# Kernel tuning notes

Hardware: AMD Instinct MI355X
Metric: run time of the kernel (lower is better)

Reference implementation:

```python
import jax, jax.numpy as jnp
import numpy as np
from jax import lax

B, N, C = 256, 256, 192
HEADS = 6
HD = C // HEADS
WIN = 16
AGENT = 49
POOL = 7            # int(agent_num ** 0.5)
SCALE = HD ** -0.5


def _pool_matrix(inn, out):
    # PyTorch AdaptiveAvgPool2d bin edges: start=floor(i*inn/out), end=ceil((i+1)*inn/out)
    P = np.zeros((out, inn), np.float32)
    for i in range(out):
        s = (i * inn) // out
        e = -(((-(i + 1)) * inn) // out)
        P[i, s:e] = 1.0 / (e - s)
    return jnp.asarray(P)

_P = _pool_matrix(WIN, POOL)  # (7, 16) adaptive-avg-pool operator


def _resize_bilinear(x, out_h, out_w):
    # matches F.interpolate(mode='bilinear', align_corners=False)
    H, W = x.shape[-2], x.shape[-1]
    def idx(out, inn):
        s = (jnp.arange(out, dtype=jnp.float32) + 0.5) * (inn / out) - 0.5
        s = jnp.maximum(s, 0.0)
        i0 = jnp.minimum(jnp.floor(s).astype(jnp.int32), inn - 1)
        i1 = jnp.minimum(i0 + 1, inn - 1)
        return i0, i1, s - i0.astype(jnp.float32)
    h0, h1, th = idx(out_h, H)
    w0, w1, tw = idx(out_w, W)
    xh = x[..., h0, :] * (1.0 - th)[:, None] + x[..., h1, :] * th[:, None]
    return xh[..., :, w0] * (1.0 - tw) + xh[..., :, w1] * tw


def setup_inputs() -> dict:
    key = jax.random.key(0)
    ks = jax.random.split(key, 18)
    lin = lambda k: jax.random.normal(k, (C, C), jnp.float32) * 0.02
    zc = jnp.zeros((C,), jnp.float32)
    tn = lambda k, shp: jax.random.normal(k, shp, jnp.float32) * 0.02
    return {
        "x_F1": jax.random.normal(ks[0], (B, N, C), jnp.float32),
        "x_C2": jax.random.normal(ks[1], (B, N, C), jnp.float32),
        "x_C1": jax.random.normal(ks[2], (B, N, C), jnp.float32),
        "Wq": lin(ks[3]), "bq": zc,
        "Wk": lin(ks[4]), "bk": zc,
        "Wv": lin(ks[5]), "bv": zc,
        "Wa1": lin(ks[6]), "ba1": zc,
        "Wa2": lin(ks[7]), "ba2": zc,
        "an_bias": tn(ks[8], (HEADS, AGENT, 7, 7)),
        "na_bias": tn(ks[9], (HEADS, AGENT, 7, 7)),
        "ah_bias": tn(ks[10], (1, HEADS, AGENT, WIN, 1)),
        "aw_bias": tn(ks[11], (1, HEADS, AGENT, 1, WIN)),
        "ha_bias": tn(ks[12], (1, HEADS, WIN, 1, AGENT)),
        "wa_bias": tn(ks[13], (1, HEADS, 1, WIN, AGENT)),
        "dwc_w": tn(ks[14], (C, 1, 3, 3)),
        "dwc_b": zc,
        "Wp": lin(ks[15]), "bp": zc,
    }


def reference(x_F1, x_C2, x_C1, Wq, bq, Wk, bk, Wv, bv, Wa1, ba1, Wa2, ba2,
              an_bias, na_bias, ah_bias, aw_bias, ha_bias, wa_bias,
              dwc_w, dwc_b, Wp, bp):
    b, n, c = x_F1.shape
    h = w = WIN
    q = x_F1 @ Wq.T + bq
    k = (x_F1 + x_C2 - x_C1) @ Wk.T + bk
    v = (x_C2 - x_C1) @ Wv.T + bv
    # agent tokens: linear -> adaptive avg pool 16x16 -> 7x7 -> (b, 49, c)
    a1 = (x_C1 @ Wa1.T + ba1).reshape(b, h, w, c)
    a1 = jnp.einsum('ph,bhwc,qw->bpqc', _P, a1, _P).reshape(b, AGENT, c)
    a2 = (x_C2 @ Wa2.T + ba2).reshape(b, h, w, c)
    a2 = jnp.einsum('ph,bhwc,qw->bpqc', _P, a2, _P).reshape(b, AGENT, c)
    qh = q.reshape(b, n, HEADS, HD).transpose(0, 2, 1, 3)
    kh = k.reshape(b, n, HEADS, HD).transpose(0, 2, 1, 3)
    vh = v.reshape(b, n, HEADS, HD).transpose(0, 2, 1, 3)
    a1h = a1.reshape(b, AGENT, HEADS, HD).transpose(0, 2, 1, 3)
    a2h = a2.reshape(b, AGENT, HEADS, HD).transpose(0, 2, 1, 3)
    # stage 1: agent <- k/v attention, bias = interp(an_bias) + (ah+aw)
    pb = (_resize_bilinear(an_bias, h, w).reshape(1, HEADS, AGENT, n)
          + (ah_bias + aw_bias).reshape(1, HEADS, AGENT, n))
    attn2 = jax.nn.softmax(SCALE * jnp.einsum('bhad,bhnd->bhan', a2h, kh) + pb, axis=-1)
    agent_v = jnp.einsum('bhan,bhnd->bhad', attn2, vh)
    # stage 2: query <- agent attention, bias = interp(na_bias)^T + (ha+wa)
    ab = (jnp.swapaxes(_resize_bilinear(na_bias, h, w).reshape(HEADS, AGENT, n), -1, -2)[None]
          + (ha_bias + wa_bias).reshape(1, HEADS, n, AGENT))
    q_attn = jax.nn.softmax(SCALE * jnp.einsum('bhnd,bhad->bhna', qh, a1h) + ab, axis=-1)
    x = jnp.einsum('bhna,bhad->bhnd', q_attn, agent_v).transpose(0, 2, 1, 3).reshape(b, n, c)
    # depthwise 3x3 conv on q as spatial map
    q_img = q.reshape(b, h, w, c).transpose(0, 3, 1, 2)
    dw = lax.conv_general_dilated(q_img, dwc_w, (1, 1), ((1, 1), (1, 1)),
                                  feature_group_count=c,
                                  dimension_numbers=('NCHW', 'OIHW', 'NCHW'))
    dw = dw + dwc_b.reshape(1, c, 1, 1)
    x = x + dw.transpose(0, 2, 3, 1).reshape(b, n, c)
    return x @ Wp.T + bp
```

## Files before the change

### kernel.cpp

```cpp
#include <hip/hip_runtime.h>

typedef __bf16 bf16;
typedef __bf16 bf16x8 __attribute__((ext_vector_type(8)));
typedef float  f32x4  __attribute__((ext_vector_type(4)));

#define DEVI __device__ __forceinline__

static constexpr int   BATCH = 256;
static constexpr int   SEQ   = 256;
static constexpr int   CH    = 192;
static constexpr int   NH    = 6;
static constexpr int   AG    = 49;
static constexpr float QK_SCALE = 0.17677669529663687f;

__device__ constexpr int   PPN[16]  = {1,1,2,1,2,1,2,1,1,2,1,2,1,2,1,1};
__device__ constexpr int   PPB0[16] = {0,0,0,1,1,2,2,3,3,3,4,4,5,5,6,6};
__device__ constexpr int   PPB1[16] = {0,0,1,0,2,0,3,0,0,4,0,5,0,6,0,0};
__device__ constexpr float PPW0[16] = {1.f/3.f,1.f/3.f,1.f/3.f,1.f/3.f,1.f/3.f,1.f/3.f,1.f/3.f,0.25f,0.25f,0.25f,
                                       1.f/3.f,1.f/3.f,1.f/3.f,1.f/3.f,1.f/3.f,1.f/3.f};
__device__ constexpr float PPW1[16] = {0.f,0.f,1.f/3.f,0.f,1.f/3.f,0.f,0.25f,0.f,0.f,1.f/3.f,
                                       0.f,1.f/3.f,0.f,1.f/3.f,0.f,0.f};

#if defined(__has_builtin)
#if __has_builtin(__builtin_amdgcn_global_load_lds)
#define HAVE_GLL 1
#endif
#endif

DEVI void gll16(const void* g, void* l, int lane) {
#ifdef HAVE_GLL
  (void)lane;
  __builtin_amdgcn_global_load_lds(
      (const __attribute__((address_space(1))) void*)g,
      (__attribute__((address_space(3))) void*)l, 16, 0, 0);
#else
  *(uint4*)((char*)l + lane * 16) = *(const uint4*)((const char*)g);
#endif
}

DEVI float bilin7(const float* m, int i, int j) {
  float sh = (i + 0.5f) * 0.4375f - 0.5f; sh = sh < 0.f ? 0.f : sh;
  float sw = (j + 0.5f) * 0.4375f - 0.5f; sw = sw < 0.f ? 0.f : sw;
  int i0 = (int)sh; if (i0 > 6) i0 = 6;
  int j0 = (int)sw; if (j0 > 6) j0 = 6;
  int i1 = i0 + 1;  if (i1 > 6) i1 = 6;
  int j1 = j0 + 1;  if (j1 > 6) j1 = 6;
  float th = sh - (float)i0, tw = sw - (float)j0;
  float v00 = m[i0*7 + j0], v01 = m[i0*7 + j1];
  float v10 = m[i1*7 + j0], v11 = m[i1*7 + j1];
  return (v00*(1.f-tw) + v01*tw)*(1.f-th) + (v10*(1.f-tw) + v11*tw)*th;
}

__global__ void k_prep(const float* Wq, const float* Wk, const float* Wv,
                       const float* Wa1, const float* Wa2, const float* Wp,
                       const float* an_bias, const float* na_bias,
                       const float* ah_bias, const float* aw_bias,
                       const float* ha_bias, const float* wa_bias,
                       bf16* wsW, float* pb, float* ab, bf16* a1, bf16* a2) {
  int gid = blockIdx.x * 256 + threadIdx.x;
  if (gid < 221184) {
    int mi = gid / 36864, r = gid - mi * 36864;
    const float* W = (mi == 0 ? Wq : mi == 1 ? Wk : mi == 2 ? Wv :
                      mi == 3 ? Wa1 : mi == 4 ? Wa2 : Wp);
    wsW[gid] = (bf16)W[r];
  } else if (gid < 296448) {
    int r = gid - 221184;
    int n = r & 255, ha = r >> 8;
    int i = n >> 4, j = n & 15;
    float val = bilin7(an_bias + (size_t)ha * 49, i, j)
              + ah_bias[ha * 16 + i] + aw_bias[ha * 16 + j];
    pb[r] = val;
  } else if (gid < 371712) {
    int r = gid - 296448;
    int a = r % 49, hn = r / 49;
    int n = hn & 255, hh = hn >> 8;
    int i = n >> 4, j = n & 15;
    float val = bilin7(na_bias + (size_t)(hh * 49 + a) * 49, i, j)
              + ha_bias[(hh * 16 + i) * 49 + a] + wa_bias[(hh * 16 + j) * 49 + a];
    ab[r] = val;
  } else if (gid < 396288) {
    int r = gid - 371712;
    if (r < 12288) a1[(size_t)12544 * CH + r] = (bf16)0.f;
    else           a2[(size_t)12544 * CH + (r - 12288)] = (bf16)0.f;
  }
}

__global__ __launch_bounds__(256) void k_combo(
    const float* xF1, const float* xC2, const float* xC1,
    bf16* f1b, bf16* kin, bf16* vin) {
  const int base = blockIdx.x * 768;
  #pragma unroll
  for (int s = 0; s < 3; ++s) {
    const int slot = base + threadIdx.x + 256 * s;
    const int row  = slot / 24;
    const int cb   = slot - row * 24;
    const size_t rf = (size_t)row * CH + cb * 8;
    float f[8], c2[8], c1[8];
    *(float4*)&f[0]  = *(const float4*)(xF1 + rf);
    *(float4*)&f[4]  = *(const float4*)(xF1 + rf + 4);
    *(float4*)&c2[0] = *(const float4*)(xC2 + rf);
    *(float4*)&c2[4] = *(const float4*)(xC2 + rf + 4);
    *(float4*)&c1[0] = *(const float4*)(xC1 + rf);
    *(float4*)&c1[4] = *(const float4*)(xC1 + rf + 4);
    bf16x8 tq, tk, tv;
    #pragma unroll
    for (int e = 0; e < 8; ++e) {
      const float d = c2[e] - c1[e];
      tq[e] = (bf16)f[e];
      tk[e] = (bf16)(f[e] + d);
      tv[e] = (bf16)d;
    }
    const size_t rowb = (size_t)row * 384;
    const int    byt  = (cb * 16) ^ ((row & 7) << 4);
    *(bf16x8*)((char*)f1b + rowb + byt) = tq;
    *(bf16x8*)((char*)kin + rowb + byt) = tk;
    *(bf16x8*)((char*)vin + rowb + byt) = tv;
  }
}

__global__ __launch_bounds__(192) void k_pool(
    const float* xC1, const float* xC2, bf16* pooled1, bf16* pooled2) {
  const int b = blockIdx.x, which = blockIdx.y, c = threadIdx.x;
  const float* src = (which ? xC2 : xC1) + (size_t)b * SEQ * CH + c;
  bf16* dst = (which ? pooled2 : pooled1) + (size_t)b * AG * CH + c;
  float acc[49];
  #pragma unroll
  for (int a = 0; a < 49; ++a) acc[a] = 0.f;
  #pragma unroll
  for (int i = 0; i < 16; ++i) {
    float jq[7] = {0.f, 0.f, 0.f, 0.f, 0.f, 0.f, 0.f};
    #pragma unroll
    for (int j = 0; j < 16; ++j) {
      const float x = src[(i * 16 + j) * CH];
      jq[PPB0[j]] += PPW0[j] * x;
      if (PPN[j] == 2) jq[PPB1[j]] += PPW1[j] * x;
    }
    {
      const int p0 = PPB0[i]; const float w0 = PPW0[i];
      #pragma unroll
      for (int qq = 0; qq < 7; ++qq) acc[p0 * 7 + qq] += w0 * jq[qq];
    }
    if (PPN[i] == 2) {
      const int p1 = PPB1[i]; const float w1 = PPW1[i];
      #pragma unroll
      for (int qq = 0; qq < 7; ++qq) acc[p1 * 7 + qq] += w1 * jq[qq];
    }
  }
  #pragma unroll
  for (int a = 0; a < 49; ++a) dst[(size_t)a * CH + c] = (bf16)acc[a];
}

__global__ __launch_bounds__(256, 3) void k_gemm3b(
    const bf16* f1b, const bf16* kin, const bf16* vin, const bf16* wsW,
    const float* bq, const float* bk, const float* bv,
    bf16* qO, bf16* kO, bf16* vO) {
  __shared__ char sA[49152] __attribute__((aligned(16)));
  const int tid = threadIdx.x, lane = tid & 63, wid = tid >> 6;
  const int l15 = lane & 15, lg = lane >> 4;
  const int wr = wid >> 1, wc = wid & 1;
  const int job = blockIdx.y;
  const int m0 = blockIdx.x * 128;
  const bf16*  Aj   = (job == 0 ? f1b : job == 1 ? kin : vin);
  const bf16*  Wj   = wsW + job * 36864;
  const float* bias = (job == 0 ? bq : job == 1 ? bk : bv);
  bf16*        outp = (job == 0 ? qO : job == 1 ? kO : vO);

  {
    const char* gsrc = (const char*)Aj + (size_t)m0 * 384;
    #pragma unroll
    for (int i = 0; i < 12; ++i) {
      const int off = (wid * 12 + i) * 1024;
      gll16(gsrc + off + lane * 16, sA + off, lane);
    }
  }
  __syncthreads();

  f32x4 acc[4][6];
  #pragma unroll
  for (int a = 0; a < 4; ++a)
    #pragma unroll
    for (int b2 = 0; b2 < 6; ++b2) acc[a][b2] = f32x4{0.f, 0.f, 0.f, 0.f};

  #pragma unroll
  for (int kk = 0; kk < 6; ++kk) {
    bf16x8 af[4];
    #pragma unroll
    for (int rt = 0; rt < 4; ++rt) {
      const int row = 64 * wr + 16 * rt + l15;
      af[rt] = *(const bf16x8*)(sA + row * 384 + ((kk * 64 + lg * 16) ^ ((row & 7) << 4)));
    }
    #pragma unroll
    for (int ct = 0; ct < 6; ++ct) {
      const int ncol = 96 * wc + 16 * ct + l15;
      bf16x8 bfr = *(const bf16x8*)&Wj[(size_t)ncol * CH + kk * 32 + 8 * lg];
      #pragma unroll
      for (int rt = 0; rt < 4; ++rt)
        acc[rt][ct] = __builtin_amdgcn_mfma_f32_16x16x32_bf16(af[rt], bfr, acc[rt][ct], 0, 0, 0);
    }
  }
  __syncthreads();
  #pragma unroll
  for (int ct = 0; ct < 6; ++ct) {
    const int col = 96 * wc + 16 * ct + l15;
    const float bb = bias[col];
    #pragma unroll
    for (int rt = 0; rt < 4; ++rt)
      #pragma unroll
      for (int r = 0; r < 4; ++r) {
        const int row = 64 * wr + 16 * rt + 4 * lg + r;
        *(bf16*)(sA + row * 384 + ((2 * col) ^ ((row & 7) << 4))) = (bf16)(acc[rt][ct][r] + bb);
      }
  }
  __syncthreads();
  #pragma unroll
  for (int g = 0; g < 12; ++g) {
    const int ch  = tid + 256 * g;
    const int row = ch / 24;
    const int y   = (ch - row * 24) * 16;
    bf16x8 vv = *(const bf16x8*)(sA + row * 384 + (y ^ ((row & 7) << 4)));
    *(bf16x8*)((char*)outp + (size_t)(m0 + row) * 384 + y) = vv;
  }
}

DEVI void gemm_body(const bf16* Asrc, const bf16* W, const float* bias,
                    bf16* outp, int m0, bf16 (*sA)[72]) {
  const int tid = threadIdx.x, lane = tid & 63, wid = tid >> 6;
  const int l15 = lane & 15, lg = lane >> 4;
  const int wr = wid >> 1, wc = wid & 1;
  const int srow = tid >> 1, shalf = tid & 1;

  f32x4 acc[4][6];
  #pragma unroll
  for (int a = 0; a < 4; ++a)
    #pragma unroll
    for (int b2 = 0; b2 < 6; ++b2) acc[a][b2] = f32x4{0.f, 0.f, 0.f, 0.f};

  for (int ks = 0; ks < 3; ++ks) {
    const int k0 = ks * 64;
    const uint4* src = (const uint4*)(Asrc + (size_t)(m0 + srow) * CH + k0 + shalf * 32);
    #pragma unroll
    for (int i2 = 0; i2 < 4; ++i2)
      *(uint4*)&sA[srow][shalf * 32 + 8 * i2] = src[i2];
    __syncthreads();
    #pragma unroll
    for (int kk = 0; kk < 64; kk += 32) {
      bf16x8 af[4];
      #pragma unroll
      for (int rt = 0; rt < 4; ++rt)
        af[rt] = *(const bf16x8*)&sA[64 * wr + 16 * rt + l15][kk + 8 * lg];
      #pragma unroll
      for (int ct = 0; ct < 6; ++ct) {
        const int ncol = 96 * wc + 16 * ct + l15;
        bf16x8 bfr = *(const bf16x8*)&W[(size_t)ncol * CH + k0 + kk + 8 * lg];
        #pragma unroll
        for (int rt = 0; rt < 4; ++rt)
          acc[rt][ct] = __builtin_amdgcn_mfma_f32_16x16x32_bf16(af[rt], bfr, acc[rt][ct], 0, 0, 0);
      }
    }
    __syncthreads();
  }
  #pragma unroll
  for (int ct = 0; ct < 6; ++ct) {
    const int col = 96 * wc + 16 * ct + l15;
    const float bb = bias[col];
    #pragma unroll
    for (int rt = 0; rt < 4; ++rt) {
      const size_t rbase = (size_t)(m0 + 64 * wr + 16 * rt + 4 * lg);
      #pragma unroll
      for (int r = 0; r < 4; ++r)
        outp[(rbase + r) * CH + col] = (bf16)(acc[rt][ct][r] + bb);
    }
  }
}

__global__ __launch_bounds__(256, 2) void k_gemm2(
    const bf16* pooled1, const bf16* pooled2, const bf16* wsW,
    const float* ba1, const float* ba2, bf16* a1, bf16* a2) {
  __shared__ bf16 sA[128][72] __attribute__((aligned(16)));
  const int m0 = blockIdx.x * 128;
  if (blockIdx.y == 0) gemm_body(pooled1, wsW + 3 * 36864, ba1, a1, m0, sA);
  else                 gemm_body(pooled2, wsW + 4 * 36864, ba2, a2, m0, sA);
}

__global__ __launch_bounds__(256, 3) void k_gemm_out(
    const bf16* xsum, const bf16* Wp, const float* bp, float* out) {
  __shared__ char sA[49152] __attribute__((aligned(16)));
  const int tid = threadIdx.x, lane = tid & 63, wid = tid >> 6;
  const int l15 = lane & 15, lg = lane >> 4;
  const int wr = wid >> 1, wc = wid & 1;
  const int m0 = blockIdx.x * 128;

  {
    const char* gsrc = (const char*)xsum + (size_t)m0 * 384;
    #pragma unroll
    for (int i = 0; i < 12; ++i) {
      const int off = (wid * 12 + i) * 1024;
      gll16(gsrc + off + lane * 16, sA + off, lane);
    }
  }
  __syncthreads();

  f32x4 acc[4][6];
  #pragma unroll
  for (int a = 0; a < 4; ++a)
    #pragma unroll
    for (int b2 = 0; b2 < 6; ++b2) acc[a][b2] = f32x4{0.f, 0.f, 0.f, 0.f};

  #pragma unroll
  for (int kk = 0; kk < 6; ++kk) {
    bf16x8 af[4];
    #pragma unroll
    for (int rt = 0; rt < 4; ++rt) {
      const int row = 64 * wr + 16 * rt + l15;
      af[rt] = *(const bf16x8*)(sA + row * 384 + ((kk * 64 + lg * 16) ^ ((row & 7) << 4)));
    }
    #pragma unroll
    for (int ct = 0; ct < 6; ++ct) {
      const int ncol = 96 * wc + 16 * ct + l15;
      bf16x8 bfr = *(const bf16x8*)&Wp[(size_t)ncol * CH + kk * 32 + 8 * lg];
      #pragma unroll
      for (int rt = 0; rt < 4; ++rt)
        acc[rt][ct] = __builtin_amdgcn_mfma_f32_16x16x32_bf16(af[rt], bfr, acc[rt][ct], 0, 0, 0);
    }
  }
  #pragma unroll
  for (int ct = 0; ct < 6; ++ct) {
    const int col = 96 * wc + 16 * ct + l15;
    const float bb = bp[col];
    #pragma unroll
    for (int rt = 0; rt < 4; ++rt)
      #pragma unroll
      for (int r = 0; r < 4; ++r)
        out[(size_t)(m0 + 64 * wr + 16 * rt + 4 * lg + r) * CH + col] = acc[rt][ct][r] + bb;
  }
}

__global__ __launch_bounds__(256, 2) void k_attn(
    const bf16* q, const bf16* k, const bf16* v,
    const bf16* a1, const bf16* a2, const float* pb, const float* ab,
    bf16* xout) {
  const int h = blockIdx.x, b = blockIdx.y;
  __shared__ char uSmem[36864] __attribute__((aligned(16)));
  bf16 (*log1)[264] = reinterpret_cast<bf16 (*)[264]>(uSmem);
  bf16 (*log2)[72]  = reinterpret_cast<bf16 (*)[72]>(uSmem);
  __shared__ bf16 sVT[32][264] __attribute__((aligned(16)));
  __shared__ bf16 sAVT[32][72] __attribute__((aligned(16)));
  __shared__ float srow1[64];
  __shared__ float srow2[256];

  const int tid = threadIdx.x, lane = tid & 63, wv = tid >> 6;
  const int l15 = lane & 15, lg = lane >> 4;

  const bf16* qb  = q  + (size_t)b * SEQ * CH + h * 32;
  const bf16* kb  = k  + (size_t)b * SEQ * CH + h * 32;
  const bf16* vb  = v  + (size_t)b * SEQ * CH + h * 32;
  const bf16* a1b = a1 + (size_t)b * AG  * CH + h * 32;
  const bf16* a2b = a2 + (size_t)b * AG  * CH + h * 32;

  {
    const int p = tid & 127, dg = tid >> 7;
    const bf16* s0 = vb + (size_t)(2 * p) * CH + dg * 16;
    bf16x8 r0a = ((const bf16x8*)s0)[0];
    bf16x8 r0b = ((const bf16x8*)s0)[1];
    bf16x8 r1a = ((const bf16x8*)(s0 + CH))[0];
    bf16x8 r1b = ((const bf16x8*)(s0 + CH))[1];
    #pragma unroll
    for (int j = 0; j < 8; ++j) {
      union { bf16 e[2]; unsigned u; } u0, u1;
      u0.e[0] = r0a[j]; u0.e[1] = r1a[j];
      u1.e[0] = r0b[j]; u1.e[1] = r1b[j];
      *(unsigned*)&sVT[dg * 16 + j][2 * p]     = u0.u;
      *(unsigned*)&sVT[dg * 16 + 8 + j][2 * p] = u1.u;
    }
  }

  {
    bf16x8 afr[4];
    #pragma unroll
    for (int rt = 0; rt < 4; ++rt)
      afr[rt] = *(const bf16x8*)(a2b + (size_t)(16 * rt + l15) * CH + 8 * lg);
    #pragma unroll
    for (int ct = 0; ct < 4; ++ct) {
      const int n = 64 * wv + 16 * ct + l15;
      bf16x8 bfr = *(const bf16x8*)(kb + (size_t)n * CH + 8 * lg);
      #pragma unroll
      for (int rt = 0; rt < 4; ++rt) {
        f32x4 acc = {0.f, 0.f, 0.f, 0.f};
        acc = __builtin_amdgcn_mfma_f32_16x16x32_bf16(afr[rt], bfr, acc, 0, 0, 0);
        #pragma unroll
        for (int r = 0; r < 4; ++r)
          log1[16 * rt + 4 * lg + r][n] = (bf16)acc[r];
      }
    }
  }
  __syncthreads();

  if (tid < 196) {
    const int a = tid >> 2, qu = tid & 3;
    const float* pbrow = pb + ((size_t)h * AG + a) * SEQ + qu * 64;
    float vbuf[64];
    float m = -1e30f;
    #pragma unroll
    for (int i2 = 0; i2 < 8; ++i2) {
      bf16x8 raw = *(const bf16x8*)&log1[a][qu * 64 + 8 * i2];
      #pragma unroll
      for (int j = 0; j < 8; ++j) {
        float x = QK_SCALE * (float)raw[j] + pbrow[8 * i2 + j];
        vbuf[8 * i2 + j] = x;
        m = fmaxf(m, x);
      }
    }
    m = fmaxf(m, __shfl_xor(m, 1));
    m = fmaxf(m, __shfl_xor(m, 2));
    float s = 0.f;
    #pragma unroll
    for (int i2 = 0; i2 < 8; ++i2) {
      bf16x8 eb;
      #pragma unroll
      for (int j = 0; j < 8; ++j) {
        float e = __expf(vbuf[8 * i2 + j] - m);
        s += e;
        eb[j] = (bf16)e;
      }
      *(bf16x8*)&log1[a][qu * 64 + 8 * i2] = eb;
    }
    s += __shfl_xor(s, 1);
    s += __shfl_xor(s, 2);
    if (qu == 0) srow1[a] = 1.f / s;
  }
  __syncthreads();

  {
    f32x4 acc0 = {0.f, 0.f, 0.f, 0.f}, acc1 = {0.f, 0.f, 0.f, 0.f};
    #pragma unroll
    for (int ksn = 0; ksn < 8; ++ksn) {
      bf16x8 af = *(const bf16x8*)&log1[16 * wv + l15][32 * ksn + 8 * lg];
      bf16x8 b0 = *(const bf16x8*)&sVT[l15][32 * ksn + 8 * lg];
      bf16x8 b1 = *(const bf16x8*)&sVT[16 + l15][32 * ksn + 8 * lg];
      acc0 = __builtin_amdgcn_mfma_f32_16x16x32_bf16(af, b0, acc0, 0, 0, 0);
      acc1 = __builtin_amdgcn_mfma_f32_16x16x32_bf16(af, b1, acc1, 0, 0, 0);
    }
    #pragma unroll
    for (int r = 0; r < 4; ++r) {
      const int a = 16 * wv + 4 * lg + r;
      const float inv = (a < AG) ? srow1[a] : 0.f;
      sAVT[l15][a]      = (bf16)(acc0[r] * inv);
      sAVT[16 + l15][a] = (bf16)(acc1[r] * inv);
    }
  }
  __syncthreads();

  {
    bf16x8 bfr[4];
    #pragma unroll
    for (int ct = 0; ct < 4; ++ct)
      bfr[ct] = *(const bf16x8*)(a1b + (size_t)(16 * ct + l15) * CH + 8 * lg);
    #pragma unroll
    for (int rt = 0; rt < 4; ++rt) {
      bf16x8 af = *(const bf16x8*)(qb + (size_t)(64 * wv + 16 * rt + l15) * CH + 8 * lg);
      #pragma unroll
      for (int ct = 0; ct < 4; ++ct) {
        f32x4 acc = {0.f, 0.f, 0.f, 0.f};
        acc = __builtin_amdgcn_mfma_f32_16x16x32_bf16(af, bfr[ct], acc, 0, 0, 0);
        #pragma unroll
        for (int r = 0; r < 4; ++r)
          log2[64 * wv + 16 * rt + 4 * lg + r][16 * ct + l15] = (bf16)acc[r];
      }
    }
  }
  __syncthreads();

  {
    const float* abrow = ab + ((size_t)h * SEQ + tid) * AG;
    float vb2[49];
    float m = -1e30f;
    #pragma unroll
    for (int i2 = 0; i2 < 6; ++i2) {
      bf16x8 raw = *(const bf16x8*)&log2[tid][8 * i2];
      #pragma unroll
      for (int j = 0; j < 8; ++j) {
        float x = QK_SCALE * (float)raw[j] + abrow[8 * i2 + j];
        vb2[8 * i2 + j] = x;
        m = fmaxf(m, x);
      }
    }
    {
      float x = QK_SCALE * (float)log2[tid][48] + abrow[48];
      vb2[48] = x;
      m = fmaxf(m, x);
    }
    float s = 0.f;
    #pragma unroll
    for (int i2 = 0; i2 < 8; ++i2) {
      bf16x8 eb;
      #pragma unroll
      for (int j = 0; j < 8; ++j) {
        const int idx = 8 * i2 + j;
        float e = 0.f;
        if (idx < AG) { e = __expf(vb2[idx] - m); }
        s += e;
        eb[j] = (bf16)e;
      }
      *(bf16x8*)&log2[tid][8 * i2] = eb;
    }
    srow2[tid] = 1.f / s;
  }
  __syncthreads();

  {
    bf16x8 bfr[2][2];
    #pragma unroll
    for (int ksn = 0; ksn < 2; ++ksn) {
      bfr[ksn][0] = *(const bf16x8*)&sAVT[l15][32 * ksn + 8 * lg];
      bfr[ksn][1] = *(const bf16x8*)&sAVT[16 + l15][32 * ksn + 8 * lg];
    }
    bf16* outp = xout + (size_t)b * SEQ * CH + h * 32;
    #pragma unroll
    for (int rt = 0; rt < 4; ++rt) {
      f32x4 acc0 = {0.f, 0.f, 0.f, 0.f}, acc1 = {0.f, 0.f, 0.f, 0.f};
      #pragma unroll
      for (int ksn = 0; ksn < 2; ++ksn) {
        bf16x8 af = *(const bf16x8*)&log2[64 * wv + 16 * rt + l15][32 * ksn + 8 * lg];
        acc0 = __builtin_amdgcn_mfma_f32_16x16x32_bf16(af, bfr[ksn][0], acc0, 0, 0, 0);
        acc1 = __builtin_amdgcn_mfma_f32_16x16x32_bf16(af, bfr[ksn][1], acc1, 0, 0, 0);
      }
      #pragma unroll
      for (int r = 0; r < 4; ++r) {
        const int nq = 64 * wv + 16 * rt + 4 * lg + r;
        const float inv = srow2[nq];
        outp[(size_t)nq * CH + l15]      = (bf16)(acc0[r] * inv);
        outp[(size_t)nq * CH + 16 + l15] = (bf16)(acc1[r] * inv);
      }
    }
  }
}

DEVI void fma8(float* acc, bf16x8 qv, float4 wa, float4 wb) {
  acc[0] += (float)qv[0] * wa.x; acc[1] += (float)qv[1] * wa.y;
  acc[2] += (float)qv[2] * wa.z; acc[3] += (float)qv[3] * wa.w;
  acc[4] += (float)qv[4] * wb.x; acc[5] += (float)qv[5] * wb.y;
  acc[6] += (float)qv[6] * wb.z; acc[7] += (float)qv[7] * wb.w;
}

__global__ __launch_bounds__(256) void k_dwconv(
    const bf16* q, const bf16* xattn, const float* dwc_w, const float* dwc_b,
    bf16* xsum) {
  __shared__ bf16 sQ[144][200] __attribute__((aligned(16)));
  __shared__ float sW[9][192] __attribute__((aligned(16)));
  const int half = blockIdx.x, b = blockIdx.y;
  const int t = threadIdx.x;
  const int base_n = half ? 112 : 0;

  if (t < 144) {
    const bf16* qs = q + ((size_t)b * SEQ + base_n + t) * CH;
    #pragma unroll
    for (int i2 = 0; i2 < 24; ++i2)
      *(uint4*)&sQ[t][8 * i2] = ((const uint4*)qs)[i2];
  }
  for (int idx = t; idx < 9 * 192; idx += 256) {
    int cc = idx / 9, tap = idx - cc * 9;
    sW[tap][cc] = dwc_w[idx];
  }
  __syncthreads();

  const int nloc = t & 127, chalf = t >> 7;
  const int n = half * 128 + nloc;
  const int ii = n >> 4, jj = n & 15;
  const bf16* xa = xattn + ((size_t)b * SEQ + n) * CH;
  char* xo = (char*)(xsum + ((size_t)b * SEQ + n) * CH);
  const int sw = (n & 7) << 4;
  const int c_base = chalf * 96;

  for (int c0 = c_base; c0 < c_base + 96; c0 += 8) {
    float accv[8];
    {
      const float4* bsrc = (const float4*)(dwc_b + c0);
      float4 b0 = bsrc[0], b1 = bsrc[1];
      accv[0] = b0.x; accv[1] = b0.y; accv[2] = b0.z; accv[3] = b0.w;
      accv[4] = b1.x; accv[5] = b1.y; accv[6] = b1.z; accv[7] = b1.w;
    }
    {
      bf16x8 xv = *(const bf16x8*)(xa + c0);
      #pragma unroll
      for (int j = 0; j < 8; ++j) accv[j] += (float)xv[j];
    }
    #pragma unroll
    for (int di = 0; di < 3; ++di) {
      const int i2 = ii + di - 1;
      if ((unsigned)i2 >= 16u) continue;
      #pragma unroll
      for (int dj = 0; dj < 3; ++dj) {
        const int j2 = jj + dj - 1;
        if ((unsigned)j2 >= 16u) continue;
        const int nn = i2 * 16 + j2 - base_n;
        bf16x8 qv = *(const bf16x8*)&sQ[nn][c0];
        const float4* wv4 = (const float4*)&sW[di * 3 + dj][c0];
        fma8(accv, qv, wv4[0], wv4[1]);
      }
    }
    bf16x8 ob;
    #pragma unroll
    for (int j = 0; j < 8; ++j) ob[j] = (bf16)accv[j];
    *(bf16x8*)(xo + ((2 * c0) ^ sw)) = ob;
  }
}

extern "C" void kernel_launch(void* const* d_in, const int* in_sizes, int n_in,
                              void* d_out, int out_size, void* d_ws, size_t ws_size,
                              hipStream_t stream) {
  (void)in_sizes; (void)n_in; (void)out_size; (void)ws_size;
  const float* xF1 = (const float*)d_in[0];
  const float* xC2 = (const float*)d_in[1];
  const float* xC1 = (const float*)d_in[2];
  const float* Wq  = (const float*)d_in[3];
  const float* bq  = (const float*)d_in[4];
  const float* Wk  = (const float*)d_in[5];
  const float* bk  = (const float*)d_in[6];
  const float* Wv  = (const float*)d_in[7];
  const float* bv  = (const float*)d_in[8];
  const float* Wa1 = (const float*)d_in[9];
  const float* ba1 = (const float*)d_in[10];
  const float* Wa2 = (const float*)d_in[11];
  const float* ba2 = (const float*)d_in[12];
  const float* an_bias = (const float*)d_in[13];
  const float* na_bias = (const float*)d_in[14];
  const float* ah_bias = (const float*)d_in[15];
  const float* aw_bias = (const float*)d_in[16];
  const float* ha_bias = (const float*)d_in[17];
  const float* wa_bias = (const float*)d_in[18];
  const float* dwc_w = (const float*)d_in[19];
  const float* dwc_b = (const float*)d_in[20];
  const float* Wp  = (const float*)d_in[21];
  const float* bp  = (const float*)d_in[22];

  char* ws = (char*)d_ws;
  size_t off = 0;
  auto nxt = [&](size_t bytes) -> char* {
    char* p = ws + off;
    off = (off + bytes + 255) & ~(size_t)255;
    return p;
  };
  const size_t XSZ = (size_t)BATCH * SEQ * CH;
  const size_t ASZ = ((size_t)BATCH * AG + 64) * CH;

  bf16*  wsW     = (bf16*)nxt(6 * 36864 * sizeof(bf16));
  float* pb      = (float*)nxt(6 * 49 * 256 * sizeof(float));
  float* ab      = (float*)nxt(6 * 256 * 49 * sizeof(float));
  bf16*  pooled1 = (bf16*)nxt(ASZ * sizeof(bf16));
  bf16*  pooled2 = (bf16*)nxt(ASZ * sizeof(bf16));
  bf16*  f1b     = (bf16*)nxt(XSZ * sizeof(bf16));
  bf16*  kin     = (bf16*)nxt(XSZ * sizeof(bf16));
  bf16*  vin     = (bf16*)nxt(XSZ * sizeof(bf16));
  bf16*  qB      = (bf16*)nxt(XSZ * sizeof(bf16));
  bf16*  kB      = (bf16*)nxt(XSZ * sizeof(bf16));
  bf16*  vB      = (bf16*)nxt(XSZ * sizeof(bf16));
  bf16*  a1B     = (bf16*)nxt(ASZ * sizeof(bf16));
  bf16*  a2B     = (bf16*)nxt(ASZ * sizeof(bf16));
  bf16*  xattn   = f1b;
  bf16*  xsum    = kin;

  k_prep<<<1548, 256, 0, stream>>>(Wq, Wk, Wv, Wa1, Wa2, Wp,
                                   an_bias, na_bias, ah_bias, aw_bias,
                                   ha_bias, wa_bias, wsW, pb, ab, a1B, a2B);
  k_combo<<<2048, 256, 0, stream>>>(xF1, xC2, xC1, f1b, kin, vin);
  k_gemm3b<<<dim3(512, 3), 256, 0, stream>>>(f1b, kin, vin, wsW, bq, bk, bv, qB, kB, vB);
  k_pool<<<dim3(BATCH, 2), 192, 0, stream>>>(xC1, xC2, pooled1, pooled2);
  k_gemm2<<<dim3(98, 2), 256, 0, stream>>>(pooled1, pooled2, wsW, ba1, ba2, a1B, a2B);
  k_attn<<<dim3(NH, BATCH), 256, 0, stream>>>(qB, kB, vB, a1B, a2B, pb, ab, xattn);
  k_dwconv<<<dim3(2, BATCH), 256, 0, stream>>>(qB, xattn, dwc_w, dwc_b, xsum);
  k_gemm_out<<<512, 256, 0, stream>>>(xsum, wsW + 5 * 36864, bp, (float*)d_out);
}
```

Measured before the change: 248.6 us.

## Fuse input combine into QKV GEMM and depthwise conv into attention

Merges the fp32-to-bf16 combine kernel with the three QKV projection GEMMs, so each block loads the raw inputs into LDS, builds q/k/v inputs there and runs all three GEMMs on 32-row tiles. This removes the intermediate bf16 buffers and their global round trip. The depthwise 3x3 conv and residual add move into the attention kernel's epilogue, per head, so the attention output is never written to global memory. The costs are smaller GEMM tiles with weight reloads from global, larger LDS per block, and uncached global reads of q neighbours in the conv.

```diff
diff --git a/kernel.cpp b/kernel.cpp
--- a/kernel.cpp
+++ b/kernel.cpp
@@ -1,6 +1,7 @@
 #include <hip/hip_runtime.h>
 
 typedef __bf16 bf16;
+typedef __bf16 bf16x4 __attribute__((ext_vector_type(4)));
 typedef __bf16 bf16x8 __attribute__((ext_vector_type(8)));
 typedef float  f32x4  __attribute__((ext_vector_type(4)));
 
@@ -85,36 +86,120 @@
   }
 }
 
-__global__ __launch_bounds__(256) void k_combo(
+__global__ __launch_bounds__(256, 2) void k_qkv(
     const float* xF1, const float* xC2, const float* xC1,
-    bf16* f1b, bf16* kin, bf16* vin) {
-  const int base = blockIdx.x * 768;
-  #pragma unroll
-  for (int s = 0; s < 3; ++s) {
-    const int slot = base + threadIdx.x + 256 * s;
-    const int row  = slot / 24;
-    const int cb   = slot - row * 24;
-    const size_t rf = (size_t)row * CH + cb * 8;
-    float f[8], c2[8], c1[8];
-    *(float4*)&f[0]  = *(const float4*)(xF1 + rf);
-    *(float4*)&f[4]  = *(const float4*)(xF1 + rf + 4);
-    *(float4*)&c2[0] = *(const float4*)(xC2 + rf);
-    *(float4*)&c2[4] = *(const float4*)(xC2 + rf + 4);
-    *(float4*)&c1[0] = *(const float4*)(xC1 + rf);
-    *(float4*)&c1[4] = *(const float4*)(xC1 + rf + 4);
-    bf16x8 tq, tk, tv;
-    #pragma unroll
-    for (int e = 0; e < 8; ++e) {
-      const float d = c2[e] - c1[e];
-      tq[e] = (bf16)f[e];
-      tk[e] = (bf16)(f[e] + d);
-      tv[e] = (bf16)d;
-    }
-    const size_t rowb = (size_t)row * 384;
-    const int    byt  = (cb * 16) ^ ((row & 7) << 4);
-    *(bf16x8*)((char*)f1b + rowb + byt) = tq;
-    *(bf16x8*)((char*)kin + rowb + byt) = tk;
-    *(bf16x8*)((char*)vin + rowb + byt) = tv;
+    const bf16* wsW, const float* bq, const float* bk, const float* bv,
+    bf16* qO, bf16* kO, bf16* vO) {
+  __shared__ char L[73728] __attribute__((aligned(16)));
+  const int tid = threadIdx.x, lane = tid & 63, wid = tid >> 6;
+  const int l15 = lane & 15, lg = lane >> 4;
+  const int m0 = blockIdx.x * 32;
+
+  {
+    const char* s0 = (const char*)(xF1 + (size_t)m0 * CH);
+    const char* s1 = (const char*)(xC2 + (size_t)m0 * CH);
+    const char* s2 = (const char*)(xC1 + (size_t)m0 * CH);
+    #pragma unroll
+    for (int i = 0; i < 6; ++i) {
+      const int off = (wid * 6 + i) * 1024;
+      gll16(s0 + off + lane * 16, L + off, lane);
+    }
+    #pragma unroll
+    for (int i = 0; i < 6; ++i) {
+      const int off = (wid * 6 + i) * 1024;
+      gll16(s1 + off + lane * 16, L + 24576 + off, lane);
+    }
+    #pragma unroll
+    for (int i = 0; i < 6; ++i) {
+      const int off = (wid * 6 + i) * 1024;
+      gll16(s2 + off + lane * 16, L + 49152 + off, lane);
+    }
+  }
+  __syncthreads();
+
+  {
+    float vF[24], v2[24], v1[24];
+    #pragma unroll
+    for (int g = 0; g < 6; ++g) {
+      const int byt = (tid + 256 * g) * 16;
+      *(float4*)&vF[4 * g] = *(const float4*)(L + byt);
+      *(float4*)&v2[4 * g] = *(const float4*)(L + 24576 + byt);
+      *(float4*)&v1[4 * g] = *(const float4*)(L + 49152 + byt);
+    }
+    __syncthreads();
+    #pragma unroll
+    for (int g = 0; g < 6; ++g) {
+      bf16x4 tq, tk, tv;
+      #pragma unroll
+      for (int e = 0; e < 4; ++e) {
+        const float f = vF[4 * g + e];
+        const float d = v2[4 * g + e] - v1[4 * g + e];
+        tq[e] = (bf16)f;
+        tk[e] = (bf16)(f + d);
+        tv[e] = (bf16)d;
+      }
+      const int f0  = (tid + 256 * g) * 4;
+      const int row = f0 / 192, col = f0 - row * 192;
+      const int cb2 = col * 2;
+      const int byt = row * 384 + ((cb2 & ~15) ^ ((row & 7) << 4)) + (cb2 & 15);
+      *(bf16x4*)(L + byt)         = tq;
+      *(bf16x4*)(L + 12288 + byt) = tk;
+      *(bf16x4*)(L + 24576 + byt) = tv;
+    }
+  }
+  __syncthreads();
+
+  #pragma unroll 1
+  for (int job = 0; job < 3; ++job) {
+    const bf16*  Wj   = wsW + job * 36864;
+    const float* bias = (job == 0 ? bq : job == 1 ? bk : bv);
+    bf16*        outp = (job == 0 ? qO : job == 1 ? kO : vO);
+    const char*  T    = L + job * 12288;
+
+    f32x4 acc[2][3];
+    #pragma unroll
+    for (int rt = 0; rt < 2; ++rt)
+      #pragma unroll
+      for (int ct = 0; ct < 3; ++ct) acc[rt][ct] = f32x4{0.f, 0.f, 0.f, 0.f};
+
+    #pragma unroll
+    for (int kk = 0; kk < 6; ++kk) {
+      bf16x8 af[2];
+      #pragma unroll
+      for (int rt = 0; rt < 2; ++rt) {
+        const int row = 16 * rt + l15;
+        af[rt] = *(const bf16x8*)(T + row * 384 + ((kk * 64 + lg * 16) ^ ((row & 7) << 4)));
+      }
+      #pragma unroll
+      for (int ct = 0; ct < 3; ++ct) {
+        const int ncol = 48 * wid + 16 * ct + l15;
+        bf16x8 bfr = *(const bf16x8*)&Wj[(size_t)ncol * CH + kk * 32 + 8 * lg];
+        acc[0][ct] = __builtin_amdgcn_mfma_f32_16x16x32_bf16(af[0], bfr, acc[0][ct], 0, 0, 0);
+        acc[1][ct] = __builtin_amdgcn_mfma_f32_16x16x32_bf16(af[1], bfr, acc[1][ct], 0, 0, 0);
+      }
+    }
+    __syncthreads();
+    #pragma unroll
+    for (int ct = 0; ct < 3; ++ct) {
+      const int col = 48 * wid + 16 * ct + l15;
+      const float bb = bias[col];
+      #pragma unroll
+      for (int rt = 0; rt < 2; ++rt)
+        #pragma unroll
+        for (int r = 0; r < 4; ++r) {
+          const int row = 16 * rt + 4 * lg + r;
+          *(bf16*)(L + 36864 + row * 400 + col * 2) = (bf16)(acc[rt][ct][r] + bb);
+        }
+    }
+    __syncthreads();
+    #pragma unroll
+    for (int v = 0; v < 3; ++v) {
+      const int c   = tid + 256 * v;
+      const int row = c / 24;
+      const int y   = (c - row * 24) * 16;
+      bf16x8 vv = *(const bf16x8*)(L + 36864 + row * 400 + y);
+      *(bf16x8*)((char*)outp + (size_t)(m0 + row) * 384 + y) = vv;
+    }
   }
 }
 
@@ -148,78 +233,6 @@
   }
   #pragma unroll
   for (int a = 0; a < 49; ++a) dst[(size_t)a * CH + c] = (bf16)acc[a];
-}
-
-__global__ __launch_bounds__(256, 3) void k_gemm3b(
-    const bf16* f1b, const bf16* kin, const bf16* vin, const bf16* wsW,
-    const float* bq, const float* bk, const float* bv,
-    bf16* qO, bf16* kO, bf16* vO) {
-  __shared__ char sA[49152] __attribute__((aligned(16)));
-  const int tid = threadIdx.x, lane = tid & 63, wid = tid >> 6;
-  const int l15 = lane & 15, lg = lane >> 4;
-  const int wr = wid >> 1, wc = wid & 1;
-  const int job = blockIdx.y;
-  const int m0 = blockIdx.x * 128;
-  const bf16*  Aj   = (job == 0 ? f1b : job == 1 ? kin : vin);
-  const bf16*  Wj   = wsW + job * 36864;
-  const float* bias = (job == 0 ? bq : job == 1 ? bk : bv);
-  bf16*        outp = (job == 0 ? qO : job == 1 ? kO : vO);
-
-  {
-    const char* gsrc = (const char*)Aj + (size_t)m0 * 384;
-    #pragma unroll
-    for (int i = 0; i < 12; ++i) {
-      const int off = (wid * 12 + i) * 1024;
-      gll16(gsrc + off + lane * 16, sA + off, lane);
-    }
-  }
-  __syncthreads();
-
-  f32x4 acc[4][6];
-  #pragma unroll
-  for (int a = 0; a < 4; ++a)
-    #pragma unroll
-    for (int b2 = 0; b2 < 6; ++b2) acc[a][b2] = f32x4{0.f, 0.f, 0.f, 0.f};
-
-  #pragma unroll
-  for (int kk = 0; kk < 6; ++kk) {
-    bf16x8 af[4];
-    #pragma unroll
-    for (int rt = 0; rt < 4; ++rt) {
-      const int row = 64 * wr + 16 * rt + l15;
-      af[rt] = *(const bf16x8*)(sA + row * 384 + ((kk * 64 + lg * 16) ^ ((row & 7) << 4)));
-    }
-    #pragma unroll
-    for (int ct = 0; ct < 6; ++ct) {
-      const int ncol = 96 * wc + 16 * ct + l15;
-      bf16x8 bfr = *(const bf16x8*)&Wj[(size_t)ncol * CH + kk * 32 + 8 * lg];
-      #pragma unroll
-      for (int rt = 0; rt < 4; ++rt)
-        acc[rt][ct] = __builtin_amdgcn_mfma_f32_16x16x32_bf16(af[rt], bfr, acc[rt][ct], 0, 0, 0);
-    }
-  }
-  __syncthreads();
-  #pragma unroll
-  for (int ct = 0; ct < 6; ++ct) {
-    const int col = 96 * wc + 16 * ct + l15;
-    const float bb = bias[col];
-    #pragma unroll
-    for (int rt = 0; rt < 4; ++rt)
-      #pragma unroll
-      for (int r = 0; r < 4; ++r) {
-        const int row = 64 * wr + 16 * rt + 4 * lg + r;
-        *(bf16*)(sA + row * 384 + ((2 * col) ^ ((row & 7) << 4))) = (bf16)(acc[rt][ct][r] + bb);
-      }
-  }
-  __syncthreads();
-  #pragma unroll
-  for (int g = 0; g < 12; ++g) {
-    const int ch  = tid + 256 * g;
-    const int row = ch / 24;
-    const int y   = (ch - row * 24) * 16;
-    bf16x8 vv = *(const bf16x8*)(sA + row * 384 + (y ^ ((row & 7) << 4)));
-    *(bf16x8*)((char*)outp + (size_t)(m0 + row) * 384 + y) = vv;
-  }
 }
 
 DEVI void gemm_body(const bf16* Asrc, const bf16* W, const float* bias,
@@ -338,7 +351,7 @@
 __global__ __launch_bounds__(256, 2) void k_attn(
     const bf16* q, const bf16* k, const bf16* v,
     const bf16* a1, const bf16* a2, const float* pb, const float* ab,
-    bf16* xout) {
+    const float* dwc_w, const float* dwc_b, bf16* xsum) {
   const int h = blockIdx.x, b = blockIdx.y;
   __shared__ char uSmem[36864] __attribute__((aligned(16)));
   bf16 (*log1)[264] = reinterpret_cast<bf16 (*)[264]>(uSmem);
@@ -347,6 +360,9 @@
   __shared__ bf16 sAVT[32][72] __attribute__((aligned(16)));
   __shared__ float srow1[64];
   __shared__ float srow2[256];
+  __shared__ bf16 xat[256][36] __attribute__((aligned(16)));
+  __shared__ float sW[9][32];
+  __shared__ float dwb[32];
 
   const int tid = threadIdx.x, lane = tid & 63, wv = tid >> 6;
   const int l15 = lane & 15, lg = lane >> 4;
@@ -356,6 +372,12 @@
   const bf16* vb  = v  + (size_t)b * SEQ * CH + h * 32;
   const bf16* a1b = a1 + (size_t)b * AG  * CH + h * 32;
   const bf16* a2b = a2 + (size_t)b * AG  * CH + h * 32;
+
+  for (int idx = tid; idx < 288; idx += 256) {
+    const int cl = idx / 9, tap = idx - cl * 9;
+    sW[tap][cl] = dwc_w[(32 * h + cl) * 9 + tap];
+  }
+  if (tid < 32) dwb[tid] = dwc_b[32 * h + tid];
 
   {
     const int p = tid & 127, dg = tid >> 7;
@@ -514,7 +536,6 @@
       bfr[ksn][0] = *(const bf16x8*)&sAVT[l15][32 * ksn + 8 * lg];
       bfr[ksn][1] = *(const bf16x8*)&sAVT[16 + l15][32 * ksn + 8 * lg];
     }
-    bf16* outp = xout + (size_t)b * SEQ * CH + h * 32;
     #pragma unroll
     for (int rt = 0; rt < 4; ++rt) {
       f32x4 acc0 = {0.f, 0.f, 0.f, 0.f}, acc1 = {0.f, 0.f, 0.f, 0.f};
@@ -528,61 +549,25 @@
       for (int r = 0; r < 4; ++r) {
         const int nq = 64 * wv + 16 * rt + 4 * lg + r;
         const float inv = srow2[nq];
-        outp[(size_t)nq * CH + l15]      = (bf16)(acc0[r] * inv);
-        outp[(size_t)nq * CH + 16 + l15] = (bf16)(acc1[r] * inv);
-      }
-    }
-  }
-}
-
-DEVI void fma8(float* acc, bf16x8 qv, float4 wa, float4 wb) {
-  acc[0] += (float)qv[0] * wa.x; acc[1] += (float)qv[1] * wa.y;
-  acc[2] += (float)qv[2] * wa.z; acc[3] += (float)qv[3] * wa.w;
-  acc[4] += (float)qv[4] * wb.x; acc[5] += (float)qv[5] * wb.y;
-  acc[6] += (float)qv[6] * wb.z; acc[7] += (float)qv[7] * wb.w;
-}
-
-__global__ __launch_bounds__(256) void k_dwconv(
-    const bf16* q, const bf16* xattn, const float* dwc_w, const float* dwc_b,
-    bf16* xsum) {
-  __shared__ bf16 sQ[144][200] __attribute__((aligned(16)));
-  __shared__ float sW[9][192] __attribute__((aligned(16)));
-  const int half = blockIdx.x, b = blockIdx.y;
-  const int t = threadIdx.x;
-  const int base_n = half ? 112 : 0;
-
-  if (t < 144) {
-    const bf16* qs = q + ((size_t)b * SEQ + base_n + t) * CH;
-    #pragma unroll
-    for (int i2 = 0; i2 < 24; ++i2)
-      *(uint4*)&sQ[t][8 * i2] = ((const uint4*)qs)[i2];
-  }
-  for (int idx = t; idx < 9 * 192; idx += 256) {
-    int cc = idx / 9, tap = idx - cc * 9;
-    sW[tap][cc] = dwc_w[idx];
-  }
-  __syncthreads();
-
-  const int nloc = t & 127, chalf = t >> 7;
-  const int n = half * 128 + nloc;
-  const int ii = n >> 4, jj = n & 15;
-  const bf16* xa = xattn + ((size_t)b * SEQ + n) * CH;
-  char* xo = (char*)(xsum + ((size_t)b * SEQ + n) * CH);
-  const int sw = (n & 7) << 4;
-  const int c_base = chalf * 96;
-
-  for (int c0 = c_base; c0 < c_base + 96; c0 += 8) {
-    float accv[8];
-    {
-      const float4* bsrc = (const float4*)(dwc_b + c0);
-      float4 b0 = bsrc[0], b1 = bsrc[1];
-      accv[0] = b0.x; accv[1] = b0.y; accv[2] = b0.z; accv[3] = b0.w;
-      accv[4] = b1.x; accv[5] = b1.y; accv[6] = b1.z; accv[7] = b1.w;
-    }
-    {
-      bf16x8 xv = *(const bf16x8*)(xa + c0);
-      #pragma unroll
-      for (int j = 0; j < 8; ++j) accv[j] += (float)xv[j];
+        xat[nq][l15]      = (bf16)(acc0[r] * inv);
+        xat[nq][16 + l15] = (bf16)(acc1[r] * inv);
+      }
+    }
+  }
+  __syncthreads();
+
+  {
+    const int n = tid, ii = n >> 4, jj = n & 15;
+    float acc[32];
+    #pragma unroll
+    for (int u = 0; u < 4; ++u) {
+      bf16x4 xa0 = *(const bf16x4*)&xat[n][8 * u];
+      bf16x4 xa1 = *(const bf16x4*)&xat[n][8 * u + 4];
+      #pragma unroll
+      for (int e = 0; e < 4; ++e) {
+        acc[8 * u + e]     = dwb[8 * u + e]     + (float)xa0[e];
+        acc[8 * u + 4 + e] = dwb[8 * u + 4 + e] + (float)xa1[e];
+      }
     }
     #pragma unroll
     for (int di = 0; di < 3; ++di) {
@@ -592,16 +577,29 @@
       for (int dj = 0; dj < 3; ++dj) {
         const int j2 = jj + dj - 1;
         if ((unsigned)j2 >= 16u) continue;
-        const int nn = i2 * 16 + j2 - base_n;
-        bf16x8 qv = *(const bf16x8*)&sQ[nn][c0];
-        const float4* wv4 = (const float4*)&sW[di * 3 + dj][c0];
-        fma8(accv, qv, wv4[0], wv4[1]);
-      }
-    }
-    bf16x8 ob;
-    #pragma unroll
-    for (int j = 0; j < 8; ++j) ob[j] = (bf16)accv[j];
-    *(bf16x8*)(xo + ((2 * c0) ^ sw)) = ob;
+        const int tap = di * 3 + dj;
+        const bf16* qr = q + ((size_t)b * SEQ + i2 * 16 + j2) * CH + h * 32;
+        #pragma unroll
+        for (int u = 0; u < 4; ++u) {
+          bf16x8 qv = *(const bf16x8*)(qr + 8 * u);
+          const float4* wv4 = (const float4*)&sW[tap][8 * u];
+          float4 wa = wv4[0], wb2 = wv4[1];
+          acc[8*u+0] += (float)qv[0] * wa.x;  acc[8*u+1] += (float)qv[1] * wa.y;
+          acc[8*u+2] += (float)qv[2] * wa.z;  acc[8*u+3] += (float)qv[3] * wa.w;
+          acc[8*u+4] += (float)qv[4] * wb2.x; acc[8*u+5] += (float)qv[5] * wb2.y;
+          acc[8*u+6] += (float)qv[6] * wb2.z; acc[8*u+7] += (float)qv[7] * wb2.w;
+        }
+      }
+    }
+    char* xo = (char*)xsum + (size_t)(b * SEQ + n) * 384;
+    const int sw = (n & 7) << 4;
+    #pragma unroll
+    for (int u = 0; u < 4; ++u) {
+      bf16x8 ob;
+      #pragma unroll
+      for (int e = 0; e < 8; ++e) ob[e] = (bf16)acc[8 * u + e];
+      *(bf16x8*)(xo + ((64 * h + 16 * u) ^ sw)) = ob;
+    }
   }
 }
 
@@ -648,25 +646,20 @@
   float* ab      = (float*)nxt(6 * 256 * 49 * sizeof(float));
   bf16*  pooled1 = (bf16*)nxt(ASZ * sizeof(bf16));
   bf16*  pooled2 = (bf16*)nxt(ASZ * sizeof(bf16));
-  bf16*  f1b     = (bf16*)nxt(XSZ * sizeof(bf16));
-  bf16*  kin     = (bf16*)nxt(XSZ * sizeof(bf16));
-  bf16*  vin     = (bf16*)nxt(XSZ * sizeof(bf16));
   bf16*  qB      = (bf16*)nxt(XSZ * sizeof(bf16));
   bf16*  kB      = (bf16*)nxt(XSZ * sizeof(bf16));
   bf16*  vB      = (bf16*)nxt(XSZ * sizeof(bf16));
   bf16*  a1B     = (bf16*)nxt(ASZ * sizeof(bf16));
   bf16*  a2B     = (bf16*)nxt(ASZ * sizeof(bf16));
-  bf16*  xattn   = f1b;
-  bf16*  xsum    = kin;
+  bf16*  xsum    = (bf16*)nxt(XSZ * sizeof(bf16));
 
   k_prep<<<1548, 256, 0, stream>>>(Wq, Wk, Wv, Wa1, Wa2, Wp,
                                    an_bias, na_bias, ah_bias, aw_bias,
                                    ha_bias, wa_bias, wsW, pb, ab, a1B, a2B);
-  k_combo<<<2048, 256, 0, stream>>>(xF1, xC2, xC1, f1b, kin, vin);
-  k_gemm3b<<<dim3(512, 3), 256, 0, stream>>>(f1b, kin, vin, wsW, bq, bk, bv, qB, kB, vB);
+  k_qkv<<<2048, 256, 0, stream>>>(xF1, xC2, xC1, wsW, bq, bk, bv, qB, kB, vB);
   k_pool<<<dim3(BATCH, 2), 192, 0, stream>>>(xC1, xC2, pooled1, pooled2);
   k_gemm2<<<dim3(98, 2), 256, 0, stream>>>(pooled1, pooled2, wsW, ba1, ba2, a1B, a2B);
-  k_attn<<<dim3(NH, BATCH), 256, 0, stream>>>(qB, kB, vB, a1B, a2B, pb, ab, xattn);
-  k_dwconv<<<dim3(2, BATCH), 256, 0, stream>>>(qB, xattn, dwc_w, dwc_b, xsum);
+  k_attn<<<dim3(NH, BATCH), 256, 0, stream>>>(qB, kB, vB, a1B, a2B, pb, ab,
+                                              dwc_w, dwc_b, xsum);
   k_gemm_out<<<512, 256, 0, stream>>>(xsum, wsW + 5 * 36864, bp, (float*)d_out);
 }
```

After: 219.3 us. 11.8% less time.
